# Kernel optimization log

Hardware: AMD Instinct MI355X
Metric: run time of the kernel (lower is better)

The kernel has to match this reference:

```python
import jax, jax.numpy as jnp
import numpy as np

EPS = 1e-16


def _grads4(x):
    """Four directional shift-differences with zero 'same' padding.

    Matches the fixed 3x3 depthwise conv kernels (cross-correlation):
      Gy: x[i-1,j]   - x[i+1,j]
      Gx: x[i,j-1]   - x[i,j+1]
      GD: x[i-1,j-1] - x[i+1,j+1]
      Gd: x[i-1,j+1] - x[i+1,j-1]
    x: [B, C, H, W]
    """
    B, C, H, W = x.shape
    xp = jnp.pad(x, ((0, 0), (0, 0), (1, 1), (1, 1)))  # zero pad like padding='same'
    gy = xp[:, :, 0:H,     1:W + 1] - xp[:, :, 2:H + 2, 1:W + 1]
    gx = xp[:, :, 1:H + 1, 0:W]     - xp[:, :, 1:H + 1, 2:W + 2]
    gD = xp[:, :, 0:H,     0:W]     - xp[:, :, 2:H + 2, 2:W + 2]
    gd = xp[:, :, 0:H,     2:W + 2] - xp[:, :, 2:H + 2, 0:W]
    return jnp.concatenate([gy, gx, gD, gd], axis=1)  # [B, 4C, H, W]


def setup_inputs() -> dict:
    key = jax.random.key(0)
    k1, k2 = jax.random.split(key)
    shape = (16, 6, 512, 512)
    outputs = jax.random.normal(k1, shape, dtype=jnp.float32)
    labels = jax.random.normal(k2, shape, dtype=jnp.float32)
    return {"outputs": outputs, "labels": labels}


def reference(outputs, labels):
    g_out = _grads4(outputs)
    g_lab = _grads4(labels)
    l1 = jnp.mean(jnp.abs(g_out - g_lab))
    return jnp.sqrt(l1 + EPS)
```

## Files before the change

kernel.cpp:

```cpp
#include <hip/hip_runtime.h>
#include <math.h>


#define NTHREADS 256
#define TROWS 16
#define SROWS (TROWS + 2)
#define WV 512
#define HT 512
#define PLANES 96
#define STRIPS_PER_PLANE (HT / TROWS)
#define TOTAL_STRIPS (PLANES * STRIPS_PER_PLANE)
#define SPB 4
#define NBLOCKS (TOTAL_STRIPS / SPB)
#define LDK 9

struct Row { float d[8]; float eL, eR; };

__device__ __forceinline__ Row lds_row(const float* __restrict__ sd,
                                       int sr, int lane) {
    Row row;
    const float4 a = *reinterpret_cast<const float4*>(sd + sr * WV + lane * 8);
    const float4 b = *reinterpret_cast<const float4*>(sd + sr * WV + lane * 8 + 4);
    row.d[0] = a.x; row.d[1] = a.y; row.d[2] = a.z; row.d[3] = a.w;
    row.d[4] = b.x; row.d[5] = b.y; row.d[6] = b.z; row.d[7] = b.w;
    const float up = __shfl_up(row.d[7], 1, 64);
    const float dn = __shfl_down(row.d[0], 1, 64);
    row.eL = (lane == 0)  ? 0.f : up;
    row.eR = (lane == 63) ? 0.f : dn;
    return row;
}

__device__ __forceinline__ void issue_loads(const float* __restrict__ out_p,
                                            const float* __restrict__ lab_p,
                                            int s, int tid,
                                            float4 (&ov)[LDK], float4 (&lv)[LDK]) {
    const int plane = s >> 5;
    const int row0  = (s & 31) * TROWS;
    const size_t pbase = (size_t)plane * (HT * WV);
    #pragma unroll
    for (int k = 0; k < LDK; ++k) {
        const int p  = tid + NTHREADS * k;
        const int r  = p >> 7;
        const int c4 = p & 127;
        const int gr = min(max(row0 + r - 1, 0), HT - 1);
        const size_t goff = pbase + (size_t)gr * WV + c4 * 4;
        ov[k] = *reinterpret_cast<const float4*>(out_p + goff);
        lv[k] = *reinterpret_cast<const float4*>(lab_p + goff);
    }
}

__device__ __forceinline__ void write_tile(float* __restrict__ sd, int s, int tid,
                                           const float4 (&ov)[LDK],
                                           const float4 (&lv)[LDK]) {
    const int row0 = (s & 31) * TROWS;
    #pragma unroll
    for (int k = 0; k < LDK; ++k) {
        const int p = tid + NTHREADS * k;
        const int r = p >> 7;
        const int gr = row0 + r - 1;
        const float m = ((unsigned)gr < (unsigned)HT) ? 1.f : 0.f;
        float4 d;
        d.x = m * (ov[k].x - lv[k].x);
        d.y = m * (ov[k].y - lv[k].y);
        d.z = m * (ov[k].z - lv[k].z);
        d.w = m * (ov[k].w - lv[k].w);
        *reinterpret_cast<float4*>(sd + (size_t)p * 4) = d;
    }
}

__device__ __forceinline__ float compute_tile(const float* __restrict__ sd,
                                              int wid, int lane) {
    float acc = 0.f;
    const int sr0 = wid * 4;
    Row rp = lds_row(sd, sr0,     lane);
    Row rc = lds_row(sd, sr0 + 1, lane);
    #pragma unroll
    for (int rr = 0; rr < 4; ++rr) {
        Row rn = lds_row(sd, sr0 + 2 + rr, lane);
        #pragma unroll
        for (int k = 0; k < 8; ++k) {
            const float cL = (k > 0) ? rc.d[k - 1] : rc.eL;
            const float cR = (k < 7) ? rc.d[k + 1] : rc.eR;
            const float pL = (k > 0) ? rp.d[k - 1] : rp.eL;
            const float pR = (k < 7) ? rp.d[k + 1] : rp.eR;
            const float nL = (k > 0) ? rn.d[k - 1] : rn.eL;
            const float nR = (k < 7) ? rn.d[k + 1] : rn.eR;

            const float gy = rp.d[k] - rn.d[k];
            const float gx = cL - cR;
            const float gD = pL - nR;
            const float gd = pR - nL;
            acc += fabsf(gy) + fabsf(gx) + fabsf(gD) + fabsf(gd);
        }
        rp = rc;
        rc = rn;
    }
    return acc;
}

__global__ __launch_bounds__(NTHREADS) void struct_loss_partial(
        const float* __restrict__ out_p, const float* __restrict__ lab_p,
        float* __restrict__ partials) {
    __shared__ float sd[SROWS * WV];

    const int tid  = threadIdx.x;
    const int wid  = tid >> 6;
    const int lane = tid & 63;
    const int s0   = blockIdx.x * SPB;

    float acc = 0.f;
    float4 ov[LDK], lv[LDK];

    issue_loads(out_p, lab_p, s0, tid, ov, lv);
    __builtin_amdgcn_sched_barrier(0);
    write_tile(sd, s0, tid, ov, lv);
    __syncthreads();

    #pragma unroll
    for (int t = 0; t < SPB; ++t) {
        if (t + 1 < SPB) {
            issue_loads(out_p, lab_p, s0 + t + 1, tid, ov, lv);
            __builtin_amdgcn_sched_barrier(0);
        }
        acc += compute_tile(sd, wid, lane);
        __syncthreads();
        if (t + 1 < SPB) {
            write_tile(sd, s0 + t + 1, tid, ov, lv);
            __syncthreads();
        }
    }

    #pragma unroll
    for (int off = 32; off > 0; off >>= 1)
        acc += __shfl_down(acc, off, 64);

    __shared__ float smem[NTHREADS / 64];
    if (lane == 0) smem[wid] = acc;
    __syncthreads();
    if (tid == 0) {
        float s = 0.f;
        #pragma unroll
        for (int w = 0; w < NTHREADS / 64; ++w) s += smem[w];
        partials[blockIdx.x] = s;
    }
}

__global__ __launch_bounds__(256) void struct_loss_final(
        const float* __restrict__ partial, float* __restrict__ out,
        int nparts, double inv_count) {
    double acc = 0.0;
    for (int i = threadIdx.x; i < nparts; i += blockDim.x)
        acc += (double)partial[i];
    #pragma unroll
    for (int off = 32; off > 0; off >>= 1)
        acc += __shfl_down(acc, off, 64);
    __shared__ double smem[4];
    const int lane = threadIdx.x & 63;
    const int wid  = threadIdx.x >> 6;
    if (lane == 0) smem[wid] = acc;
    __syncthreads();
    if (threadIdx.x == 0) {
        double s = smem[0] + smem[1] + smem[2] + smem[3];
        out[0] = (float)sqrt(s * inv_count + 1e-16);
    }
}

extern "C" void kernel_launch(void* const* d_in, const int* in_sizes, int n_in,
                              void* d_out, int out_size, void* d_ws, size_t ws_size,
                              hipStream_t stream) {
    const float* outputs = (const float*)d_in[0];
    const float* labels  = (const float*)d_in[1];
    float* out = (float*)d_out;
    float* partials = (float*)d_ws;

    const double inv_count = 1.0 / (16.0 * 24.0 * 512.0 * 512.0);

    struct_loss_partial<<<NBLOCKS, NTHREADS, 0, stream>>>(outputs, labels, partials);
    struct_loss_final<<<1, 256, 0, stream>>>(partials, out, NBLOCKS, inv_count);
}
```

Before: 40.16 us.

## Use ring-buffered LDS slots so consecutive strips reuse halo rows

Each block now handles four vertically contiguous strips of one plane and keeps an 18-row circular LDS buffer. Each later strip loads only 16 new rows instead of 18, so the two halo rows already held in LDS are reused. This cuts global reads of the halo rows by about 11% after the first strip. In exchange it adds modulo slot-index arithmetic.

```diff
diff --git a/kernel.cpp b/kernel.cpp
--- a/kernel.cpp
+++ b/kernel.cpp
@@ -4,23 +4,24 @@
 
 #define NTHREADS 256
 #define TROWS 16
-#define SROWS (TROWS + 2)
+#define SLOTS 18
 #define WV 512
 #define HT 512
 #define PLANES 96
-#define STRIPS_PER_PLANE (HT / TROWS)
-#define TOTAL_STRIPS (PLANES * STRIPS_PER_PLANE)
 #define SPB 4
-#define NBLOCKS (TOTAL_STRIPS / SPB)
-#define LDK 9
+#define BAND (SPB * TROWS)
+#define BLOCKS_PER_PLANE (HT / BAND)
+#define NBLOCKS (PLANES * BLOCKS_PER_PLANE)
+#define LDK_PRO 9
+#define LDK 8
 
 struct Row { float d[8]; float eL, eR; };
 
 __device__ __forceinline__ Row lds_row(const float* __restrict__ sd,
-                                       int sr, int lane) {
+                                       int slot, int lane) {
     Row row;
-    const float4 a = *reinterpret_cast<const float4*>(sd + sr * WV + lane * 8);
-    const float4 b = *reinterpret_cast<const float4*>(sd + sr * WV + lane * 8 + 4);
+    const float4 a = *reinterpret_cast<const float4*>(sd + slot * WV + lane * 8);
+    const float4 b = *reinterpret_cast<const float4*>(sd + slot * WV + lane * 8 + 4);
     row.d[0] = a.x; row.d[1] = a.y; row.d[2] = a.z; row.d[3] = a.w;
     row.d[4] = b.x; row.d[5] = b.y; row.d[6] = b.z; row.d[7] = b.w;
     const float up = __shfl_up(row.d[7], 1, 64);
@@ -30,102 +31,125 @@
     return row;
 }
 
-__device__ __forceinline__ void issue_loads(const float* __restrict__ out_p,
-                                            const float* __restrict__ lab_p,
-                                            int s, int tid,
-                                            float4 (&ov)[LDK], float4 (&lv)[LDK]) {
-    const int plane = s >> 5;
-    const int row0  = (s & 31) * TROWS;
-    const size_t pbase = (size_t)plane * (HT * WV);
-    #pragma unroll
-    for (int k = 0; k < LDK; ++k) {
-        const int p  = tid + NTHREADS * k;
-        const int r  = p >> 7;
-        const int c4 = p & 127;
-        const int gr = min(max(row0 + r - 1, 0), HT - 1);
-        const size_t goff = pbase + (size_t)gr * WV + c4 * 4;
-        ov[k] = *reinterpret_cast<const float4*>(out_p + goff);
-        lv[k] = *reinterpret_cast<const float4*>(lab_p + goff);
-    }
-}
-
-__device__ __forceinline__ void write_tile(float* __restrict__ sd, int s, int tid,
-                                           const float4 (&ov)[LDK],
-                                           const float4 (&lv)[LDK]) {
-    const int row0 = (s & 31) * TROWS;
-    #pragma unroll
-    for (int k = 0; k < LDK; ++k) {
-        const int p = tid + NTHREADS * k;
-        const int r = p >> 7;
-        const int gr = row0 + r - 1;
-        const float m = ((unsigned)gr < (unsigned)HT) ? 1.f : 0.f;
-        float4 d;
-        d.x = m * (ov[k].x - lv[k].x);
-        d.y = m * (ov[k].y - lv[k].y);
-        d.z = m * (ov[k].z - lv[k].z);
-        d.w = m * (ov[k].w - lv[k].w);
-        *reinterpret_cast<float4*>(sd + (size_t)p * 4) = d;
-    }
-}
-
-__device__ __forceinline__ float compute_tile(const float* __restrict__ sd,
-                                              int wid, int lane) {
-    float acc = 0.f;
-    const int sr0 = wid * 4;
-    Row rp = lds_row(sd, sr0,     lane);
-    Row rc = lds_row(sd, sr0 + 1, lane);
-    #pragma unroll
-    for (int rr = 0; rr < 4; ++rr) {
-        Row rn = lds_row(sd, sr0 + 2 + rr, lane);
-        #pragma unroll
-        for (int k = 0; k < 8; ++k) {
-            const float cL = (k > 0) ? rc.d[k - 1] : rc.eL;
-            const float cR = (k < 7) ? rc.d[k + 1] : rc.eR;
-            const float pL = (k > 0) ? rp.d[k - 1] : rp.eL;
-            const float pR = (k < 7) ? rp.d[k + 1] : rp.eR;
-            const float nL = (k > 0) ? rn.d[k - 1] : rn.eL;
-            const float nR = (k < 7) ? rn.d[k + 1] : rn.eR;
-
-            const float gy = rp.d[k] - rn.d[k];
-            const float gx = cL - cR;
-            const float gD = pL - nR;
-            const float gd = pR - nL;
-            acc += fabsf(gy) + fabsf(gx) + fabsf(gD) + fabsf(gd);
-        }
-        rp = rc;
-        rc = rn;
-    }
-    return acc;
+__device__ __forceinline__ float stencil(const Row& rp, const Row& rc,
+                                         const Row& rn) {
+    float a = 0.f;
+    #pragma unroll
+    for (int k = 0; k < 8; ++k) {
+        const float cL = (k > 0) ? rc.d[k - 1] : rc.eL;
+        const float cR = (k < 7) ? rc.d[k + 1] : rc.eR;
+        const float pL = (k > 0) ? rp.d[k - 1] : rp.eL;
+        const float pR = (k < 7) ? rp.d[k + 1] : rp.eR;
+        const float nL = (k > 0) ? rn.d[k - 1] : rn.eL;
+        const float nR = (k < 7) ? rn.d[k + 1] : rn.eR;
+
+        const float gy = rp.d[k] - rn.d[k];
+        const float gx = cL - cR;
+        const float gD = pL - nR;
+        const float gd = pR - nL;
+        a += fabsf(gy) + fabsf(gx) + fabsf(gD) + fabsf(gd);
+    }
+    return a;
 }
 
 __global__ __launch_bounds__(NTHREADS) void struct_loss_partial(
         const float* __restrict__ out_p, const float* __restrict__ lab_p,
         float* __restrict__ partials) {
-    __shared__ float sd[SROWS * WV];
+    __shared__ float sd[SLOTS * WV];
 
     const int tid  = threadIdx.x;
     const int wid  = tid >> 6;
     const int lane = tid & 63;
-    const int s0   = blockIdx.x * SPB;
+    const int plane = blockIdx.x >> 3;
+    const int S0    = (blockIdx.x & (BLOCKS_PER_PLANE - 1)) * BAND;
+    const int sbase = S0 % SLOTS;
+    const size_t pbase = (size_t)plane * (HT * WV);
+
+    {
+        float4 ov[LDK_PRO], lv[LDK_PRO];
+        #pragma unroll
+        for (int k = 0; k < LDK_PRO; ++k) {
+            const int p  = tid + NTHREADS * k;
+            const int r  = p >> 7;
+            const int c4 = p & 127;
+            const int g  = S0 - 1 + r;
+            const int gc = max(g, 0);
+            const size_t goff = pbase + (size_t)gc * WV + c4 * 4;
+            ov[k] = *reinterpret_cast<const float4*>(out_p + goff);
+            lv[k] = *reinterpret_cast<const float4*>(lab_p + goff);
+        }
+        #pragma unroll
+        for (int k = 0; k < LDK_PRO; ++k) {
+            const int p  = tid + NTHREADS * k;
+            const int r  = p >> 7;
+            const int c4 = p & 127;
+            const int g  = S0 - 1 + r;
+            const float m = (g >= 0) ? 1.f : 0.f;
+            int slot = sbase + r; if (slot >= SLOTS) slot -= SLOTS;
+            float4 d;
+            d.x = m * (ov[k].x - lv[k].x);
+            d.y = m * (ov[k].y - lv[k].y);
+            d.z = m * (ov[k].z - lv[k].z);
+            d.w = m * (ov[k].w - lv[k].w);
+            *reinterpret_cast<float4*>(sd + slot * WV + c4 * 4) = d;
+        }
+    }
+    __syncthreads();
 
     float acc = 0.f;
     float4 ov[LDK], lv[LDK];
 
-    issue_loads(out_p, lab_p, s0, tid, ov, lv);
-    __builtin_amdgcn_sched_barrier(0);
-    write_tile(sd, s0, tid, ov, lv);
-    __syncthreads();
-
     #pragma unroll
     for (int t = 0; t < SPB; ++t) {
+        const int R0 = S0 + t * TROWS;
+
         if (t + 1 < SPB) {
-            issue_loads(out_p, lab_p, s0 + t + 1, tid, ov, lv);
+            #pragma unroll
+            for (int k = 0; k < LDK; ++k) {
+                const int p  = tid + NTHREADS * k;
+                const int r  = p >> 7;
+                const int c4 = p & 127;
+                const int g  = R0 + 17 + r;
+                const int gc = min(g, HT - 1);
+                const size_t goff = pbase + (size_t)gc * WV + c4 * 4;
+                ov[k] = *reinterpret_cast<const float4*>(out_p + goff);
+                lv[k] = *reinterpret_cast<const float4*>(lab_p + goff);
+            }
             __builtin_amdgcn_sched_barrier(0);
         }
-        acc += compute_tile(sd, wid, lane);
+
+        {
+            const int m0 = (sbase + 16 * t + 4 * wid) % SLOTS;
+            int s_c = m0 + 1; if (s_c >= SLOTS) s_c -= SLOTS;
+            Row rp = lds_row(sd, m0, lane);
+            Row rc = lds_row(sd, s_c, lane);
+            #pragma unroll
+            for (int rr = 0; rr < 4; ++rr) {
+                int s_n = m0 + 2 + rr; if (s_n >= SLOTS) s_n -= SLOTS;
+                Row rn = lds_row(sd, s_n, lane);
+                acc += stencil(rp, rc, rn);
+                rp = rc;
+                rc = rn;
+            }
+        }
         __syncthreads();
+
         if (t + 1 < SPB) {
-            write_tile(sd, s0 + t + 1, tid, ov, lv);
+            #pragma unroll
+            for (int k = 0; k < LDK; ++k) {
+                const int p  = tid + NTHREADS * k;
+                const int r  = p >> 7;
+                const int c4 = p & 127;
+                const int g  = R0 + 17 + r;
+                const float m = (g < HT) ? 1.f : 0.f;
+                int slot = (sbase + 16 * t + r) % SLOTS;
+                float4 d;
+                d.x = m * (ov[k].x - lv[k].x);
+                d.y = m * (ov[k].y - lv[k].y);
+                d.z = m * (ov[k].z - lv[k].z);
+                d.w = m * (ov[k].w - lv[k].w);
+                *reinterpret_cast<float4*>(sd + slot * WV + c4 * 4) = d;
+            }
             __syncthreads();
         }
     }
```

Result: faster. 38.41 us (median of 2 runs) (-4.4%).
